# Optimization experiments

Hardware: AMD Instinct MI355X
Metric: run time of the kernel (lower is better)

Reference implementation:

```python
import jax, jax.numpy as jnp
import numpy as np

U = 50  # lstm units

def lstm_seq(x, Wx, Wh, b):
    # x: [B,S,D] -> h: [B,S,U], Keras LSTMCell gate order i,f,g,o
    B = x.shape[0]
    xz = jnp.einsum('bsd,dk->bsk', x, Wx) + b  # [B,S,4U]
    def step(carry, zt):
        h, c = carry
        z = zt + h @ Wh
        i, f, g, o = jnp.split(z, 4, axis=-1)
        c = jax.nn.sigmoid(f) * c + jax.nn.sigmoid(i) * jnp.tanh(g)
        h = jax.nn.sigmoid(o) * jnp.tanh(c)
        return (h, c), h
    init = (jnp.zeros((B, U), x.dtype), jnp.zeros((B, U), x.dtype))
    _, hs = jax.lax.scan(step, init, jnp.swapaxes(xz, 0, 1))
    return jnp.swapaxes(hs, 0, 1)

def bilstm(x, fWx, fWh, fb, bWx, bWh, bb):
    # Keras RNN(go_backwards=True) does NOT re-reverse outputs; concat as-is.
    fw = lstm_seq(x, fWx, fWh, fb)
    bw = lstm_seq(x[:, ::-1, :], bWx, bWh, bb)
    return jnp.concatenate([fw, bw], axis=-1)

def local_inference(x1e, m1, x2e, m2):
    # Literal translation: inputs are batch-first [B,S,D]; the TF code transposes
    # to [S,B,D] and batch-matmuls over the leading (seq) axis, so attention is
    # over the batch index at each timestep. A[s,i,j] = x1e[i,s]. x2e[j,s]
    A = jnp.einsum('isd,jsd->sij', x1e, x2e)
    m1t = m1.T  # [S,B]
    m2t = m2.T
    w2 = jnp.exp(A - jnp.max(A, axis=2, keepdims=True)) * m2t[:, None, :]
    alpha = w2 / (jnp.sum(w2, axis=-1, keepdims=True) + 1e-8)
    x1_dual = jnp.einsum('sij,jsd->isd', alpha, x2e)  # [B,S,D]
    A1 = A - jnp.max(A, axis=1, keepdims=True)
    w1 = jnp.exp(jnp.swapaxes(A1, 1, 2)) * m1t[:, None, :]
    beta = w1 / (jnp.sum(w1, axis=-1, keepdims=True) + 1e-8)
    x2_dual = jnp.einsum('sji,isd->jsd', beta, x1e)  # [B,S,D]
    return x1_dual, x2_dual

def esim_forward(x1, x2, emb, b1f_Wx, b1f_Wh, b1f_b, b1b_Wx, b1b_Wh, b1b_b,
                 dense_W, dense_b, b2f_Wx, b2f_Wh, b2f_b, b2b_Wx, b2b_Wh, b2b_b,
                 dense1_W, dense1_b, out_W, out_b):
    m1 = (x1 != 0).astype(jnp.float32)
    m2 = (x2 != 0).astype(jnp.float32)
    e1 = emb[x1] * m1[..., None]
    e2 = emb[x2] * m2[..., None]
    enc1 = bilstm(e1, b1f_Wx, b1f_Wh, b1f_b, b1b_Wx, b1b_Wh, b1b_b) * m1[..., None]
    enc2 = bilstm(e2, b1f_Wx, b1f_Wh, b1f_b, b1b_Wx, b1b_Wh, b1b_b) * m2[..., None]
    d1, d2 = local_inference(enc1, m1, enc2, m2)
    match1 = jnp.concatenate([enc1, d1, enc1 * d1, enc1 - d1], axis=2)
    match2 = jnp.concatenate([enc2, d2, enc2 * d2, enc2 - d2], axis=2)
    map1 = jax.nn.relu(match1 @ dense_W + dense_b)
    map2 = jax.nn.relu(match2 @ dense_W + dense_b)
    cmp1 = bilstm(map1, b2f_Wx, b2f_Wh, b2f_b, b2b_Wx, b2b_Wh, b2b_b)
    cmp2 = bilstm(map2, b2f_Wx, b2f_Wh, b2f_b, b2b_Wx, b2b_Wh, b2b_b)
    c1m = cmp1 * m1[..., None]
    c2m = cmp2 * m2[..., None]
    p1_sum = jnp.sum(c1m, axis=1) / jnp.sum(m1, axis=1)[:, None]
    p1_max = jnp.max(c1m, axis=1)
    p2_sum = jnp.sum(c2m, axis=1) / jnp.sum(m2, axis=1)[:, None]
    p2_max = jnp.max(c2m, axis=1)
    logit = jnp.concatenate([p1_sum, p1_max, p2_sum, p2_max], axis=1)
    logit = jnp.tanh(logit @ dense1_W + dense1_b)
    logit = logit @ out_W + out_b
    return jax.nn.softmax(logit, axis=-1)

def setup_inputs() -> dict:
    key = jax.random.key(0)
    ks = jax.random.split(key, 24)
    B, S, V, E = 128, 512, 20000, 50
    def w(k, shape, s=0.05):
        return jax.random.normal(k, shape, dtype=jnp.float32) * s
    return {
        'x1': jax.random.randint(ks[0], (B, S), 0, V, dtype=jnp.int32),
        'x2': jax.random.randint(ks[1], (B, S), 0, V, dtype=jnp.int32),
        'emb': jax.random.uniform(ks[2], (V, E), jnp.float32, -0.05, 0.05),
        'b1f_Wx': w(ks[3], (E, 4 * U)), 'b1f_Wh': w(ks[4], (U, 4 * U)), 'b1f_b': w(ks[5], (4 * U,)),
        'b1b_Wx': w(ks[6], (E, 4 * U)), 'b1b_Wh': w(ks[7], (U, 4 * U)), 'b1b_b': w(ks[8], (4 * U,)),
        'dense_W': w(ks[9], (400, 100), 0.02), 'dense_b': jnp.zeros((100,), jnp.float32),
        'b2f_Wx': w(ks[10], (100, 4 * U)), 'b2f_Wh': w(ks[11], (U, 4 * U)), 'b2f_b': w(ks[12], (4 * U,)),
        'b2b_Wx': w(ks[13], (100, 4 * U)), 'b2b_Wh': w(ks[14], (U, 4 * U)), 'b2b_b': w(ks[15], (4 * U,)),
        'dense1_W': w(ks[16], (400, 100), 0.02), 'dense1_b': jnp.zeros((100,), jnp.float32),
        'out_W': w(ks[17], (100, 2), 0.02), 'out_b': jnp.zeros((2,), jnp.float32),
    }

def reference(x1, x2, emb, b1f_Wx, b1f_Wh, b1f_b, b1b_Wx, b1b_Wh, b1b_b,
              dense_W, dense_b, b2f_Wx, b2f_Wh, b2f_b, b2b_Wx, b2b_Wh, b2b_b,
              dense1_W, dense1_b, out_W, out_b):
    return esim_forward(x1, x2, emb, b1f_Wx, b1f_Wh, b1f_b, b1b_Wx, b1b_Wh, b1b_b,
                        dense_W, dense_b, b2f_Wx, b2f_Wh, b2f_b, b2b_Wx, b2b_Wh, b2b_b,
                        dense1_W, dense1_b, out_W, out_b)
```

## Files before the change

### kernel.cpp

```cpp
#include <hip/hip_runtime.h>

#define TOKN 65536
#define SQ 512
#define BB 128
#define DD 100
#define APAD 132

typedef unsigned short bf16t;
typedef __attribute__((ext_vector_type(8))) short bf16x8;
typedef __attribute__((ext_vector_type(4))) float floatx4;
typedef __attribute__((ext_vector_type(2))) _Float16 half2t;

__device__ __forceinline__ float bf2f(bf16t v) {
  unsigned u = ((unsigned)v) << 16;
  return __uint_as_float(u);
}
__device__ __forceinline__ bf16t f2bf(float x) {
  unsigned u = __float_as_uint(x);
  unsigned r = u + 0x7FFFu + ((u >> 16) & 1u);
  return (bf16t)(r >> 16);
}
__device__ __forceinline__ float2 ldpair(const float* p) { return *(const float2*)p; }
__device__ __forceinline__ float2 ldpair(const bf16t* p) {
  unsigned u = *(const unsigned*)p;
  float2 r;
  r.x = __uint_as_float(u << 16);
  r.y = __uint_as_float(u & 0xFFFF0000u);
  return r;
}
__device__ __forceinline__ half2t u2h2(unsigned u) {
  union { unsigned u; half2t h; } x; x.u = u; return x.h;
}

__device__ __forceinline__ float sigm(float x) { return 1.f / (1.f + __expf(-x)); }
__device__ __forceinline__ float tanhx(float x) { return 1.f - 2.f / (1.f + __expf(2.f * x)); }

#if __has_builtin(__builtin_amdgcn_fdot2)
#define DOT2(hu, wu, acc) acc = __builtin_amdgcn_fdot2(u2h2(hu), u2h2(wu), acc, false);
#else
#define DOT2(hu, wu, acc) { half2t hh = u2h2(hu), ww = u2h2(wu); \
  acc = fmaf((float)hh[0], (float)ww[0], acc); \
  acc = fmaf((float)hh[1], (float)ww[1], acc); }
#endif

__global__ __launch_bounds__(256) void embed_kernel(
    const int* __restrict__ x1, const int* __restrict__ x2,
    const float* __restrict__ emb,
    bf16t* __restrict__ e1, bf16t* __restrict__ e2,
    float* __restrict__ m1, float* __restrict__ m2) {
  const int which = blockIdx.y;
  const int* __restrict__ x = which ? x2 : x1;
  bf16t* __restrict__ e = which ? e2 : e1;
  float* __restrict__ m = which ? m2 : m1;
  int idx = blockIdx.x * 256 + threadIdx.x;
  int t = idx >> 6, d = idx & 63;
  int tok = x[t];
  float mk = (tok != 0) ? 1.f : 0.f;
  float v = (d < 50) ? emb[tok * 50 + d] * mk : 0.f;
  e[idx] = f2bf(v);
  if (d == 0) m[t] = mk;
}

__global__ __launch_bounds__(256) void wprep_kernel(
    const float* __restrict__ w1f, const float* __restrict__ w1b,
    const float* __restrict__ w2f, const float* __restrict__ w2b,
    const float* __restrict__ dW,
    const float* __restrict__ h1f, const float* __restrict__ h1b,
    const float* __restrict__ h2f, const float* __restrict__ h2b,
    bf16t* __restrict__ w1T, bf16t* __restrict__ w2T, bf16t* __restrict__ wdT,
    unsigned* __restrict__ whP) {
  int idx = blockIdx.x * 256 + threadIdx.x;
  int sec = blockIdx.y;
  if (sec == 0) {
    if (idx >= 2 * 208 * 64) return;
    int d = idx / (208 * 64), r = idx % (208 * 64);
    int n = r >> 6, k = r & 63;
    const float* W = d ? w1b : w1f;
    float v = (n < 200 && k < 50) ? W[k * 200 + n] : 0.f;
    w1T[idx] = f2bf(v);
  } else if (sec == 1) {
    if (idx >= 2 * 208 * 128) return;
    int d = idx / (208 * 128), r = idx % (208 * 128);
    int n = r >> 7, k = r & 127;
    const float* W = d ? w2b : w2f;
    float v = (n < 200 && k < 100) ? W[k * 200 + n] : 0.f;
    w2T[idx] = f2bf(v);
  } else if (sec == 2) {
    if (idx >= 128 * 384) return;
    int n = idx / 384, kv = idx % 384;
    int reg = kv >> 7, kk = kv & 127;
    float v = 0.f;
    if (n < 100 && kk < 100) {
      if (reg == 0) v = dW[kk * 100 + n] + dW[(300 + kk) * 100 + n];
      else if (reg == 1) v = dW[(100 + kk) * 100 + n] - dW[(300 + kk) * 100 + n];
      else v = dW[(200 + kk) * 100 + n];
    }
    wdT[idx] = f2bf(v);
  } else {
    if (idx >= 4 * 25 * 200) return;
    int sd = idx / 5000, r = idx % 5000;
    int k2 = r / 200, colx = r % 200;
    const float* W = (sd == 0) ? h1f : (sd == 1) ? h1b : (sd == 2) ? h2f : h2b;
    float v0 = W[(2 * k2) * 200 + colx];
    float v1 = W[(2 * k2 + 1) * 200 + colx];
    union { _Float16 h[2]; unsigned u; } p;
    p.h[0] = (_Float16)v0;
    p.h[1] = (_Float16)v1;
    whP[idx] = p.u;
  }
}

template <int KP>
__global__ __launch_bounds__(256) void xz_mfma(
    const bf16t* __restrict__ A1, const bf16t* __restrict__ A2,
    const bf16t* __restrict__ WT,
    const float* __restrict__ bf_, const float* __restrict__ bb_,
    bf16t* __restrict__ out) {
  const int combo = blockIdx.y;
  const bf16t* __restrict__ A = (combo < 2) ? A1 : A2;
  const bf16t* __restrict__ W = WT + (size_t)(combo & 1) * 208 * KP;
  const float* __restrict__ bias = (combo & 1) ? bb_ : bf_;
  bf16t* __restrict__ O = out + (size_t)combo * TOKN * 200;
  const int tid = threadIdx.x;
  const int wave = tid >> 6, lane = tid & 63;
  const int m0 = blockIdx.x * 64 + wave * 16;
  const int l15 = lane & 15, quad = lane >> 4;
  floatx4 acc[13];
#pragma unroll
  for (int nt = 0; nt < 13; ++nt) acc[nt] = (floatx4){0.f, 0.f, 0.f, 0.f};
  const bf16t* __restrict__ arow = A + (size_t)(m0 + l15) * KP + quad * 8;
  const bf16t* __restrict__ wb = W + (size_t)l15 * KP + quad * 8;
#pragma unroll
  for (int ks = 0; ks < KP / 32; ++ks) {
    bf16x8 a = *(const bf16x8*)(arow + ks * 32);
#pragma unroll
    for (int nt = 0; nt < 13; ++nt) {
      bf16x8 b = *(const bf16x8*)(wb + (size_t)nt * 16 * KP + ks * 32);
      acc[nt] = __builtin_amdgcn_mfma_f32_16x16x32_bf16(a, b, acc[nt], 0, 0, 0);
    }
  }
  const int crow = m0 + quad * 4;
#pragma unroll
  for (int nt = 0; nt < 13; ++nt) {
    int n = nt * 16 + l15;
    if (n < 200) {
      float bn = bias[n];
#pragma unroll
      for (int r = 0; r < 4; ++r)
        O[(size_t)(crow + r) * 200 + n] = f2bf(acc[nt][r] + bn);
    }
  }
}

__global__ __launch_bounds__(256) void dense_mfma(
    const bf16t* __restrict__ enc1, const bf16t* __restrict__ enc2,
    const bf16t* __restrict__ d1b, const bf16t* __restrict__ d2b,
    const bf16t* __restrict__ wdT, const float* __restrict__ bias,
    bf16t* __restrict__ map1, bf16t* __restrict__ map2) {
  const int inp = blockIdx.y;
  const bf16t* __restrict__ E = inp ? enc2 : enc1;
  const bf16t* __restrict__ Db = inp ? d2b : d1b;
  bf16t* __restrict__ O = inp ? map2 : map1;
  const int tid = threadIdx.x;
  const int wave = tid >> 6, lane = tid & 63;
  const int m0 = blockIdx.x * 64 + wave * 16;
  const int l15 = lane & 15, quad = lane >> 4;
  floatx4 acc[8];
#pragma unroll
  for (int nt = 0; nt < 8; ++nt) acc[nt] = (floatx4){0.f, 0.f, 0.f, 0.f};
  const bf16t* __restrict__ erow = E + (size_t)(m0 + l15) * 128 + quad * 8;
  const bf16t* __restrict__ drow = Db + (size_t)(m0 + l15) * 128 + quad * 8;
  const bf16t* __restrict__ wb = wdT + (size_t)l15 * 384 + quad * 8;
#pragma unroll
  for (int ks = 0; ks < 4; ++ks) {
    bf16x8 ae = *(const bf16x8*)(erow + ks * 32);
    bf16x8 ad = *(const bf16x8*)(drow + ks * 32);
    bf16x8 aed;
#pragma unroll
    for (int q = 0; q < 8; ++q) {
      float pe = bf2f((bf16t)ae[q]);
      float pd = bf2f((bf16t)ad[q]);
      aed[q] = (short)f2bf(pe * pd);
    }
#pragma unroll
    for (int nt = 0; nt < 8; ++nt) {
      const bf16t* wn = wb + (size_t)nt * 16 * 384 + ks * 32;
      bf16x8 b0 = *(const bf16x8*)(wn);
      acc[nt] = __builtin_amdgcn_mfma_f32_16x16x32_bf16(ae, b0, acc[nt], 0, 0, 0);
      bf16x8 b1 = *(const bf16x8*)(wn + 128);
      acc[nt] = __builtin_amdgcn_mfma_f32_16x16x32_bf16(ad, b1, acc[nt], 0, 0, 0);
      bf16x8 b2 = *(const bf16x8*)(wn + 256);
      acc[nt] = __builtin_amdgcn_mfma_f32_16x16x32_bf16(aed, b2, acc[nt], 0, 0, 0);
    }
  }
  const int crow = m0 + quad * 4;
#pragma unroll
  for (int nt = 0; nt < 8; ++nt) {
    int n = nt * 16 + l15;
    float bn = (n < 100) ? bias[n] : 0.f;
#pragma unroll
    for (int r = 0; r < 4; ++r) {
      float v = (n < 100) ? fmaxf(acc[nt][r] + bn, 0.f) : 0.f;
      O[(size_t)(crow + r) * 128 + n] = f2bf(v);
    }
  }
}

__global__ __launch_bounds__(256, 2) void lstm_scan(
    const bf16t* __restrict__ xz,
    const unsigned* __restrict__ whPL,
    bf16t* __restrict__ out1, bf16t* __restrict__ out2,
    const float* __restrict__ m1, const float* __restrict__ m2,
    int hasMask) {
  const int blk = blockIdx.x;
  const int scan = blk >> 7;
  const int b = blk & 127;
  const int inp = scan >> 1;
  const int dir = scan & 1;
  const bf16t* __restrict__ xzs = xz + (size_t)scan * TOKN * 200 + (size_t)b * SQ * 200;
  bf16t* __restrict__ outRaw = (inp ? out2 : out1) + (size_t)b * SQ * 128;
  bf16t* __restrict__ outp = outRaw + dir * 50;
  const float* __restrict__ mk = (inp ? m2 : m1) + b * SQ;

  const int tid = threadIdx.x;
  const int lane = tid & 63;
  const int u = tid >> 2, g = tid & 3;
  const int col = g * 50 + u;
  __shared__ __align__(16) unsigned hbuf[2][32];

  const unsigned* __restrict__ wsrc = whPL + dir * 5000;
  const int colc = (tid < 200) ? col : 0;
  unsigned wreg[25];
#pragma unroll
  for (int k2 = 0; k2 < 25; ++k2) wreg[k2] = wsrc[k2 * 200 + colc];
#pragma unroll
  for (int k2 = 0; k2 < 25; ++k2) asm volatile("" : "+v"(wreg[k2]));

  if (tid < 64) ((unsigned*)hbuf)[tid] = 0;
  float c = 0.f;
  float z0 = 0.f, z1 = 0.f;
  if (tid < 200) {
    z0 = bf2f(xzs[(size_t)(dir ? (SQ - 1) : 0) * 200 + col]);
    z1 = bf2f(xzs[(size_t)(dir ? (SQ - 2) : 1) * 200 + col]);
  }
  __syncthreads();
  for (int t = 0; t < SQ; ++t) {
    int tp = (t + 2 < SQ) ? (t + 2) : (SQ - 1);
    int rowp = dir ? (SQ - 1 - tp) : tp;
    float znext = 0.f;
    if (tid < 200) {
      znext = bf2f(xzs[(size_t)rowp * 200 + col]);
      const uint4* hp = (const uint4*)&hbuf[t & 1][0];
      uint4 q0 = hp[0], q1 = hp[1], q2 = hp[2], q3 = hp[3], q4 = hp[4], q5 = hp[5];
      unsigned qL = hbuf[t & 1][24];
      float za = z0, zb = 0.f, zc = 0.f, zd = 0.f;
      DOT2(q0.x, wreg[0], za)  DOT2(q0.y, wreg[1], zb)
      DOT2(q0.z, wreg[2], zc)  DOT2(q0.w, wreg[3], zd)
      DOT2(q1.x, wreg[4], za)  DOT2(q1.y, wreg[5], zb)
      DOT2(q1.z, wreg[6], zc)  DOT2(q1.w, wreg[7], zd)
      DOT2(q2.x, wreg[8], za)  DOT2(q2.y, wreg[9], zb)
      DOT2(q2.z, wreg[10], zc) DOT2(q2.w, wreg[11], zd)
      DOT2(q3.x, wreg[12], za) DOT2(q3.y, wreg[13], zb)
      DOT2(q3.z, wreg[14], zc) DOT2(q3.w, wreg[15], zd)
      DOT2(q4.x, wreg[16], za) DOT2(q4.y, wreg[17], zb)
      DOT2(q4.z, wreg[18], zc) DOT2(q4.w, wreg[19], zd)
      DOT2(q5.x, wreg[20], za) DOT2(q5.y, wreg[21], zb)
      DOT2(q5.z, wreg[22], zc) DOT2(q5.w, wreg[23], zd)
      DOT2(qL,   wreg[24], za)
      float z = (za + zb) + (zc + zd);
      float a = (g == 2) ? tanhx(z) : sigm(z);
      int base = lane & ~3;
      if (g == 0) {
        float af = __shfl(a, base + 1);
        float ag_ = __shfl(a, base + 2);
        float ao = __shfl(a, base + 3);
        c = af * c + a * ag_;
        float hn = ao * tanhx(c);
        ((_Float16*)&hbuf[(t + 1) & 1][0])[u] = (_Float16)hn;
        float mv = hasMask ? mk[t] : 1.f;
        outp[(size_t)t * 128 + u] = f2bf(hn * mv);
      }
    } else if (dir == 0 && tid < 214) {
      *(unsigned*)&outRaw[(size_t)t * 128 + 100 + 2 * (tid - 200)] = 0u;
    }
    __syncthreads();
    z0 = z1;
    z1 = znext;
  }
}

__global__ __launch_bounds__(256) void attn_kernel(
    const bf16t* __restrict__ enc1, const bf16t* __restrict__ enc2,
    const float* __restrict__ m1, const float* __restrict__ m2,
    bf16t* __restrict__ d1b, bf16t* __restrict__ d2b) {
  const int s = blockIdx.x;
  const int tid = threadIdx.x;
  __shared__ __align__(16) float E1[BB][DD];
  __shared__ __align__(16) float E2[BB + 1][DD];
  __shared__ __align__(16) float Ah[64][APAD];
  __shared__ float mk1[BB], mk2[BB];
  __shared__ float rden[64];

  for (int idx = tid; idx < BB * 50; idx += 256) {
    int i = idx / 50, dp = idx - i * 50;
    float2 v1 = ldpair(enc1 + ((size_t)i * SQ + s) * 128 + 2 * dp);
    E1[i][2 * dp] = v1.x;
    E1[i][2 * dp + 1] = v1.y;
    float2 v2 = ldpair(enc2 + ((size_t)i * SQ + s) * 128 + 2 * dp);
    E2[i][2 * dp] = v2.x;
    E2[i][2 * dp + 1] = v2.y;
  }
  if (tid < BB) {
    mk1[tid] = m1[tid * SQ + s];
    mk2[tid] = m2[tid * SQ + s];
  }
  __syncthreads();

  const int ti = tid >> 4, tjj = tid & 15;
  const int xj = tid & 127;
  const int xd0 = (tid >> 7) * 50;
  float N[50];
#pragma unroll
  for (int q = 0; q < 50; ++q) N[q] = 0.f;
  float Dacc = 0.f, M = -1e30f;

  for (int half = 0; half < 2; ++half) {
    const int r0 = half * 64;
    float acc[4][8];
#pragma unroll
    for (int ii = 0; ii < 4; ++ii)
#pragma unroll
      for (int jj = 0; jj < 8; ++jj) acc[ii][jj] = 0.f;
    for (int k = 0; k < DD; k += 4) {
      float4 a4[4], b4[8];
#pragma unroll
      for (int ii = 0; ii < 4; ++ii)
        a4[ii] = *(const float4*)&E1[r0 + 4 * ti + ii][k];
#pragma unroll
      for (int jj = 0; jj < 8; ++jj)
        b4[jj] = *(const float4*)&E2[tjj + 16 * jj][k];
#pragma unroll
      for (int ii = 0; ii < 4; ++ii)
#pragma unroll
        for (int jj = 0; jj < 8; ++jj)
          acc[ii][jj] += a4[ii].x * b4[jj].x + a4[ii].y * b4[jj].y +
                         a4[ii].z * b4[jj].z + a4[ii].w * b4[jj].w;
    }
#pragma unroll
    for (int ii = 0; ii < 4; ++ii)
#pragma unroll
      for (int jj = 0; jj < 8; ++jj)
        Ah[4 * ti + ii][tjj + 16 * jj] = acc[ii][jj];
    __syncthreads();

    {
      float lm = M;
      for (int i = 0; i < 64; ++i) lm = fmaxf(lm, Ah[i][xj]);
      float scale = __expf(M - lm);
      Dacc *= scale;
#pragma unroll
      for (int q = 0; q < 50; ++q) N[q] *= scale;
      for (int i = 0; i < 64; ++i) {
        float p = __expf(Ah[i][xj] - lm) * mk1[r0 + i];
        Dacc += p;
        const float2* e1p = (const float2*)&E1[r0 + i][xd0];
#pragma unroll
        for (int q = 0; q < 25; ++q) {
          float2 ev = e1p[q];
          N[2 * q] += p * ev.x;
          N[2 * q + 1] += p * ev.y;
        }
      }
      M = lm;
    }
    __syncthreads();

    {
      int row = tid >> 2, seg = tid & 3;
      float mx = -1e30f;
      for (int q = 0; q < 32; ++q) mx = fmaxf(mx, Ah[row][seg + 4 * q]);
      mx = fmaxf(mx, __shfl_xor(mx, 1));
      mx = fmaxf(mx, __shfl_xor(mx, 2));
      float sm = 0.f;
      for (int q = 0; q < 32; ++q) {
        int jc = seg + 4 * q;
        float p = __expf(Ah[row][jc] - mx) * mk2[jc];
        Ah[row][jc] = p;
        sm += p;
      }
      sm += __shfl_xor(sm, 1);
      sm += __shfl_xor(sm, 2);
      if (seg == 0) rden[row] = sm + 1e-8f;
    }
    __syncthreads();

    {
      float o[4][8];
#pragma unroll
      for (int ii = 0; ii < 4; ++ii)
#pragma unroll
        for (int jj = 0; jj < 8; ++jj) o[ii][jj] = 0.f;
      for (int jb = 0; jb < BB; ++jb) {
        float pv[4], ev[8];
#pragma unroll
        for (int ii = 0; ii < 4; ++ii) pv[ii] = Ah[4 * ti + ii][jb];
#pragma unroll
        for (int jj = 0; jj < 8; ++jj) ev[jj] = E2[jb][tjj + 16 * jj];
#pragma unroll
        for (int ii = 0; ii < 4; ++ii)
#pragma unroll
          for (int jj = 0; jj < 8; ++jj) o[ii][jj] += pv[ii] * ev[jj];
      }
#pragma unroll
      for (int ii = 0; ii < 4; ++ii) {
        int i = r0 + 4 * ti + ii;
        float inv = 1.f / rden[4 * ti + ii];
#pragma unroll
        for (int jj = 0; jj < 8; ++jj) {
          int d = tjj + 16 * jj;
          float val = (d < DD) ? o[ii][jj] * inv : 0.f;
          d1b[((size_t)i * SQ + s) * 128 + d] = f2bf(val);
        }
      }
    }
    __syncthreads();
  }
  float invD = 1.f / (Dacc + 1e-8f);
#pragma unroll
  for (int q = 0; q < 50; ++q)
    d2b[((size_t)xj * SQ + s) * 128 + xd0 + q] = f2bf(N[q] * invD);
  if (xd0 == 50) {
#pragma unroll
    for (int q = 0; q < 28; ++q)
      d2b[((size_t)xj * SQ + s) * 128 + 100 + q] = 0;
  }
}

__global__ __launch_bounds__(128) void pool_kernel(
    const bf16t* __restrict__ cmp1, const bf16t* __restrict__ cmp2,
    const float* __restrict__ m1, const float* __restrict__ m2,
    float* __restrict__ pooled) {
  int b = blockIdx.x & 127, inp = blockIdx.x >> 7;
  const bf16t* C = (inp ? cmp2 : cmp1) + (size_t)b * SQ * 128;
  const float* M = (inp ? m2 : m1) + b * SQ;
  int f = threadIdx.x;
  float ms = 0.f;
  for (int s = f; s < SQ; s += 128) ms += M[s];
  __shared__ float red[128];
  red[f] = ms;
  __syncthreads();
  for (int o = 64; o > 0; o >>= 1) {
    if (f < o) red[f] += red[f + o];
    __syncthreads();
  }
  float msum = red[0];
  if (f < 100) {
    float sm = 0.f, mx = -1e30f;
    for (int s = 0; s < SQ; ++s) {
      float v = bf2f(C[(size_t)s * 128 + f]) * M[s];
      sm += v;
      mx = fmaxf(mx, v);
    }
    pooled[b * 400 + inp * 200 + f] = sm / msum;
    pooled[b * 400 + inp * 200 + 100 + f] = mx;
  }
}

__global__ __launch_bounds__(128) void final_kernel(
    const float* __restrict__ pooled, const float* __restrict__ W1,
    const float* __restrict__ b1, const float* __restrict__ W2,
    const float* __restrict__ b2, float* __restrict__ out) {
  int b = blockIdx.x;
  int j = threadIdx.x;
  __shared__ float pr[400];
  __shared__ float h[100];
  for (int idx = j; idx < 400; idx += 128) pr[idx] = pooled[b * 400 + idx];
  __syncthreads();
  if (j < 100) {
    float a = b1[j];
    for (int k = 0; k < 400; ++k) a += pr[k] * W1[k * 100 + j];
    h[j] = tanhx(a);
  }
  __syncthreads();
  if (j == 0) {
    float l0 = b2[0], l1 = b2[1];
    for (int k = 0; k < 100; ++k) {
      l0 += h[k] * W2[k * 2];
      l1 += h[k] * W2[k * 2 + 1];
    }
    float mx = fmaxf(l0, l1);
    float e0 = __expf(l0 - mx), e1 = __expf(l1 - mx);
    float inv = 1.f / (e0 + e1);
    out[b * 2] = e0 * inv;
    out[b * 2 + 1] = e1 * inv;
  }
}

extern "C" void kernel_launch(void* const* d_in, const int* in_sizes, int n_in,
                              void* d_out, int out_size, void* d_ws, size_t ws_size,
                              hipStream_t stream) {
  const int* x1 = (const int*)d_in[0];
  const int* x2 = (const int*)d_in[1];
  const float* emb = (const float*)d_in[2];
  const float* b1f_Wx = (const float*)d_in[3];
  const float* b1f_Wh = (const float*)d_in[4];
  const float* b1f_b = (const float*)d_in[5];
  const float* b1b_Wx = (const float*)d_in[6];
  const float* b1b_Wh = (const float*)d_in[7];
  const float* b1b_b = (const float*)d_in[8];
  const float* dense_W = (const float*)d_in[9];
  const float* dense_b = (const float*)d_in[10];
  const float* b2f_Wx = (const float*)d_in[11];
  const float* b2f_Wh = (const float*)d_in[12];
  const float* b2f_b = (const float*)d_in[13];
  const float* b2b_Wx = (const float*)d_in[14];
  const float* b2b_Wh = (const float*)d_in[15];
  const float* b2b_b = (const float*)d_in[16];
  const float* dense1_W = (const float*)d_in[17];
  const float* dense1_b = (const float*)d_in[18];
  const float* out_W = (const float*)d_in[19];
  const float* out_b = (const float*)d_in[20];
  float* out = (float*)d_out;

  char* base = (char*)d_ws;
  bf16t* xz = (bf16t*)base;
  bf16t* d1b = (bf16t*)base;
  bf16t* d2b = d1b + (size_t)TOKN * 128;
  char* r1 = base + (size_t)4 * TOKN * 200 * 2;
  bf16t* enc1 = (bf16t*)r1;
  bf16t* enc2 = enc1 + (size_t)TOKN * 128;
  bf16t* e1b = (bf16t*)r1;
  bf16t* e2b = e1b + (size_t)TOKN * 64;
  char* r2 = r1 + (size_t)2 * TOKN * 128 * 2;
  bf16t* map1 = (bf16t*)r2;
  bf16t* map2 = map1 + (size_t)TOKN * 128;
  char* r3 = r2 + (size_t)2 * TOKN * 128 * 2;
  float* m1 = (float*)r3;
  float* m2 = m1 + TOKN;
  float* pooled = m2 + TOKN;
  bf16t* w1T = (bf16t*)(r3 + ((size_t)2 * TOKN + 128 * 400) * 4);
  bf16t* w2T = w1T + 2 * 208 * 64;
  bf16t* wdT = w2T + 2 * 208 * 128;
  unsigned* whP = (unsigned*)(wdT + 128 * 384);
  bf16t* cmp1 = enc1;
  bf16t* cmp2 = enc2;
  (void)in_sizes; (void)n_in; (void)out_size; (void)ws_size;

  embed_kernel<<<dim3(TOKN * 64 / 256, 2), 256, 0, stream>>>(
      x1, x2, emb, e1b, e2b, m1, m2);
  wprep_kernel<<<dim3(208, 4), 256, 0, stream>>>(
      b1f_Wx, b1b_Wx, b2f_Wx, b2b_Wx, dense_W,
      b1f_Wh, b1b_Wh, b2f_Wh, b2b_Wh, w1T, w2T, wdT, whP);
  xz_mfma<64><<<dim3(TOKN / 64, 4), 256, 0, stream>>>(
      e1b, e2b, w1T, b1f_b, b1b_b, xz);
  lstm_scan<<<512, 256, 0, stream>>>(xz, whP, enc1, enc2, m1, m2, 1);
  attn_kernel<<<SQ, 256, 0, stream>>>(enc1, enc2, m1, m2, d1b, d2b);
  dense_mfma<<<dim3(TOKN / 64, 2), 256, 0, stream>>>(
      enc1, enc2, d1b, d2b, wdT, dense_b, map1, map2);
  xz_mfma<128><<<dim3(TOKN / 64, 4), 256, 0, stream>>>(
      map1, map2, w2T, b2f_b, b2b_b, xz);
  lstm_scan<<<512, 256, 0, stream>>>(xz, whP + 2 * 5000, cmp1, cmp2, m1, m2, 0);
  pool_kernel<<<256, 128, 0, stream>>>(cmp1, cmp2, m1, m2, pooled);
  final_kernel<<<128, 128, 0, stream>>>(pooled, dense1_W, dense1_b, out_W, out_b, out);
}
```

Before: 1.243 ms.

## Transpose xz to time-contiguous layout and batch LSTM scan loads per eight steps

The xz projection is now written time-major per (scan, batch, column), so each LSTM thread fetches eight timesteps of its gate preactivation in one 16-byte load. Mask loads and output stores are also batched per eight steps instead of once per step. The per-step zeroing of pad columns moves out of the serial scan into a separate padzero kernel. The goal is fewer scattered global accesses on the latency-bound recurrence, at the cost of strided uint2 writes in xz_mfma and one extra launch.

```diff
diff --git a/kernel.cpp b/kernel.cpp
--- a/kernel.cpp
+++ b/kernel.cpp
@@ -59,6 +59,15 @@
   float v = (d < 50) ? emb[tok * 50 + d] * mk : 0.f;
   e[idx] = f2bf(v);
   if (d == 0) m[t] = mk;
+}
+
+__global__ __launch_bounds__(256) void padzero_kernel(
+    unsigned* __restrict__ p1, unsigned* __restrict__ p2) {
+  int idx = blockIdx.x * 256 + threadIdx.x;
+  if (idx >= TOKN * 14) return;
+  int t = idx / 14, d = idx - t * 14;
+  p1[(size_t)t * 64 + 50 + d] = 0u;
+  p2[(size_t)t * 64 + 50 + d] = 0u;
 }
 
 __global__ __launch_bounds__(256) void wprep_kernel(
@@ -140,14 +149,17 @@
     }
   }
   const int crow = m0 + quad * 4;
+  const int bidx = crow >> 9;
+  const int trow = crow & 511;
 #pragma unroll
   for (int nt = 0; nt < 13; ++nt) {
     int n = nt * 16 + l15;
     if (n < 200) {
       float bn = bias[n];
-#pragma unroll
-      for (int r = 0; r < 4; ++r)
-        O[(size_t)(crow + r) * 200 + n] = f2bf(acc[nt][r] + bn);
+      union { bf16t h[4]; uint2 u2; } pk;
+#pragma unroll
+      for (int r = 0; r < 4; ++r) pk.h[r] = f2bf(acc[nt][r] + bn);
+      *(uint2*)&O[((size_t)bidx * 200 + n) * SQ + trow] = pk.u2;
     }
   }
 }
@@ -206,8 +218,13 @@
   }
 }
 
+#define WLIST(X) X(0) X(1) X(2) X(3) X(4) X(5) X(6) X(7) X(8) X(9) X(10) X(11) \
+  X(12) X(13) X(14) X(15) X(16) X(17) X(18) X(19) X(20) X(21) X(22) X(23) X(24)
+#define WDECL(i) unsigned w##i = wsrc[i * 200 + colc];
+#define WPIN(i) asm volatile("" : "+v"(w##i));
+
 __global__ __launch_bounds__(256, 2) void lstm_scan(
-    const bf16t* __restrict__ xz,
+    const bf16t* __restrict__ xzT,
     const unsigned* __restrict__ whPL,
     bf16t* __restrict__ out1, bf16t* __restrict__ out2,
     const float* __restrict__ m1, const float* __restrict__ m2,
@@ -217,75 +234,105 @@
   const int b = blk & 127;
   const int inp = scan >> 1;
   const int dir = scan & 1;
-  const bf16t* __restrict__ xzs = xz + (size_t)scan * TOKN * 200 + (size_t)b * SQ * 200;
-  bf16t* __restrict__ outRaw = (inp ? out2 : out1) + (size_t)b * SQ * 128;
-  bf16t* __restrict__ outp = outRaw + dir * 50;
-  const float* __restrict__ mk = (inp ? m2 : m1) + b * SQ;
-
   const int tid = threadIdx.x;
   const int lane = tid & 63;
   const int u = tid >> 2, g = tid & 3;
   const int col = g * 50 + u;
+  const bool active = (tid < 200);
+  const int colc = active ? col : 0;
+  const bf16t* __restrict__ xcol =
+      xzT + (((size_t)scan * 128 + b) * 200 + colc) * SQ;
+  bf16t* __restrict__ outp = (inp ? out2 : out1) + (size_t)b * SQ * 128 + dir * 50;
+  const float* __restrict__ mk = (inp ? m2 : m1) + b * SQ;
   __shared__ __align__(16) unsigned hbuf[2][32];
 
   const unsigned* __restrict__ wsrc = whPL + dir * 5000;
-  const int colc = (tid < 200) ? col : 0;
-  unsigned wreg[25];
-#pragma unroll
-  for (int k2 = 0; k2 < 25; ++k2) wreg[k2] = wsrc[k2 * 200 + colc];
-#pragma unroll
-  for (int k2 = 0; k2 < 25; ++k2) asm volatile("" : "+v"(wreg[k2]));
+  WLIST(WDECL)
+  WLIST(WPIN)
 
   if (tid < 64) ((unsigned*)hbuf)[tid] = 0;
   float c = 0.f;
-  float z0 = 0.f, z1 = 0.f;
-  if (tid < 200) {
-    z0 = bf2f(xzs[(size_t)(dir ? (SQ - 1) : 0) * 200 + col]);
-    z1 = bf2f(xzs[(size_t)(dir ? (SQ - 2) : 1) * 200 + col]);
+  const bool msk = hasMask && active && (g == 0);
+  const float4* mk4 = (const float4*)mk;
+
+  uint4 zcur, znxt;
+  {
+    int r0 = dir ? (SQ - 8) : 0;
+    int r1 = dir ? (SQ - 16) : 8;
+    zcur = *(const uint4*)(xcol + r0);
+    znxt = *(const uint4*)(xcol + r1);
   }
   __syncthreads();
-  for (int t = 0; t < SQ; ++t) {
-    int tp = (t + 2 < SQ) ? (t + 2) : (SQ - 1);
-    int rowp = dir ? (SQ - 1 - tp) : tp;
-    float znext = 0.f;
-    if (tid < 200) {
-      znext = bf2f(xzs[(size_t)rowp * 200 + col]);
-      const uint4* hp = (const uint4*)&hbuf[t & 1][0];
+
+  for (int g8 = 0; g8 < SQ / 8; ++g8) {
+    float zf[8];
+    {
+      unsigned d0 = zcur.x, d1 = zcur.y, d2 = zcur.z, d3 = zcur.w;
+      zf[0] = __uint_as_float(d0 << 16);
+      zf[1] = __uint_as_float(d0 & 0xFFFF0000u);
+      zf[2] = __uint_as_float(d1 << 16);
+      zf[3] = __uint_as_float(d1 & 0xFFFF0000u);
+      zf[4] = __uint_as_float(d2 << 16);
+      zf[5] = __uint_as_float(d2 & 0xFFFF0000u);
+      zf[6] = __uint_as_float(d3 << 16);
+      zf[7] = __uint_as_float(d3 & 0xFFFF0000u);
+    }
+    uint4 zfol = znxt;
+    {
+      int gnext = (g8 + 2 < SQ / 8) ? (g8 + 2) : (SQ / 8 - 1);
+      int rn = dir ? (SQ - 8 - 8 * gnext) : (8 * gnext);
+      znxt = *(const uint4*)(xcol + rn);
+    }
+    float mva[8];
+    if (msk) {
+      float4 ma = mk4[2 * g8], mb = mk4[2 * g8 + 1];
+      mva[0] = ma.x; mva[1] = ma.y; mva[2] = ma.z; mva[3] = ma.w;
+      mva[4] = mb.x; mva[5] = mb.y; mva[6] = mb.z; mva[7] = mb.w;
+    }
+    bf16t hsave[8];
+#pragma unroll
+    for (int j = 0; j < 8; ++j) {
+      const int par = j & 1;
+      float z0v = dir ? zf[7 - j] : zf[j];
+      const uint4* hp = (const uint4*)&hbuf[par][0];
       uint4 q0 = hp[0], q1 = hp[1], q2 = hp[2], q3 = hp[3], q4 = hp[4], q5 = hp[5];
-      unsigned qL = hbuf[t & 1][24];
-      float za = z0, zb = 0.f, zc = 0.f, zd = 0.f;
-      DOT2(q0.x, wreg[0], za)  DOT2(q0.y, wreg[1], zb)
-      DOT2(q0.z, wreg[2], zc)  DOT2(q0.w, wreg[3], zd)
-      DOT2(q1.x, wreg[4], za)  DOT2(q1.y, wreg[5], zb)
-      DOT2(q1.z, wreg[6], zc)  DOT2(q1.w, wreg[7], zd)
-      DOT2(q2.x, wreg[8], za)  DOT2(q2.y, wreg[9], zb)
-      DOT2(q2.z, wreg[10], zc) DOT2(q2.w, wreg[11], zd)
-      DOT2(q3.x, wreg[12], za) DOT2(q3.y, wreg[13], zb)
-      DOT2(q3.z, wreg[14], zc) DOT2(q3.w, wreg[15], zd)
-      DOT2(q4.x, wreg[16], za) DOT2(q4.y, wreg[17], zb)
-      DOT2(q4.z, wreg[18], zc) DOT2(q4.w, wreg[19], zd)
-      DOT2(q5.x, wreg[20], za) DOT2(q5.y, wreg[21], zb)
-      DOT2(q5.z, wreg[22], zc) DOT2(q5.w, wreg[23], zd)
-      DOT2(qL,   wreg[24], za)
-      float z = (za + zb) + (zc + zd);
-      float a = (g == 2) ? tanhx(z) : sigm(z);
+      unsigned qL = hbuf[par][24];
+      float za = z0v, zb = 0.f, zc = 0.f, zd = 0.f;
+      DOT2(q0.x, w0, za)  DOT2(q0.y, w1, zb)
+      DOT2(q0.z, w2, zc)  DOT2(q0.w, w3, zd)
+      DOT2(q1.x, w4, za)  DOT2(q1.y, w5, zb)
+      DOT2(q1.z, w6, zc)  DOT2(q1.w, w7, zd)
+      DOT2(q2.x, w8, za)  DOT2(q2.y, w9, zb)
+      DOT2(q2.z, w10, zc) DOT2(q2.w, w11, zd)
+      DOT2(q3.x, w12, za) DOT2(q3.y, w13, zb)
+      DOT2(q3.z, w14, zc) DOT2(q3.w, w15, zd)
+      DOT2(q4.x, w16, za) DOT2(q4.y, w17, zb)
+      DOT2(q4.z, w18, zc) DOT2(q4.w, w19, zd)
+      DOT2(q5.x, w20, za) DOT2(q5.y, w21, zb)
+      DOT2(q5.z, w22, zc) DOT2(q5.w, w23, zd)
+      DOT2(qL,   w24, za)
+      float zv = (za + zb) + (zc + zd);
+      float a = (g == 2) ? tanhx(zv) : sigm(zv);
       int base = lane & ~3;
-      if (g == 0) {
-        float af = __shfl(a, base + 1);
-        float ag_ = __shfl(a, base + 2);
-        float ao = __shfl(a, base + 3);
+      float af = __shfl(a, base + 1);
+      float ag_ = __shfl(a, base + 2);
+      float ao = __shfl(a, base + 3);
+      if (active && g == 0) {
         c = af * c + a * ag_;
         float hn = ao * tanhx(c);
-        ((_Float16*)&hbuf[(t + 1) & 1][0])[u] = (_Float16)hn;
-        float mv = hasMask ? mk[t] : 1.f;
-        outp[(size_t)t * 128 + u] = f2bf(hn * mv);
+        ((_Float16*)&hbuf[par ^ 1][0])[u] = (_Float16)hn;
+        float mv = hasMask ? mva[j] : 1.f;
+        hsave[j] = f2bf(hn * mv);
       }
-    } else if (dir == 0 && tid < 214) {
-      *(unsigned*)&outRaw[(size_t)t * 128 + 100 + 2 * (tid - 200)] = 0u;
-    }
-    __syncthreads();
-    z0 = z1;
-    z1 = znext;
+      __syncthreads();
+    }
+    if (active && g == 0) {
+      int t0 = 8 * g8;
+#pragma unroll
+      for (int j = 0; j < 8; ++j)
+        outp[(size_t)(t0 + j) * 128 + u] = hsave[j];
+    }
+    zcur = zfol;
   }
 }
 
@@ -553,6 +600,8 @@
       b1f_Wh, b1b_Wh, b2f_Wh, b2b_Wh, w1T, w2T, wdT, whP);
   xz_mfma<64><<<dim3(TOKN / 64, 4), 256, 0, stream>>>(
       e1b, e2b, w1T, b1f_b, b1b_b, xz);
+  padzero_kernel<<<(TOKN * 14 + 255) / 256, 256, 0, stream>>>(
+      (unsigned*)enc1, (unsigned*)enc2);
   lstm_scan<<<512, 256, 0, stream>>>(xz, whP, enc1, enc2, m1, m2, 1);
   attn_kernel<<<SQ, 256, 0, stream>>>(enc1, enc2, m1, m2, d1b, d2b);
   dense_mfma<<<dim3(TOKN / 64, 2), 256, 0, stream>>>(
```

Result: faster. 1.139 ms (-8.3%).
